# Performance work log

Measured on AMD Instinct MI355X. Metric: run time of the kernel, lower is better.

## Reference

```python
import jax, jax.numpy as jnp
import numpy as np

B, S, E = 2, 2048, 2048
H, HKV, D = 32, 8, 64  # n_heads, n_kv_heads, head_dim


def _rope(x, cos, sin):
    # x: [B,S,h,D]; cos/sin: [1,S,1,D//2]. Complex rotate on (even,odd) pairs.
    xp = x.reshape(*x.shape[:-1], D // 2, 2)
    x0, x1 = xp[..., 0], xp[..., 1]
    r0 = x0 * cos - x1 * sin
    r1 = x0 * sin + x1 * cos
    return jnp.stack([r0, r1], axis=-1).reshape(x.shape)


def setup_inputs() -> dict:
    key = jax.random.key(0)
    ks = jax.random.split(key, 8)
    sc = 0.02
    # real RoPE frequencies (theta=10000) for realism
    inv = 1.0 / (10000.0 ** (np.arange(0, D, 2, dtype=np.float32) / D))
    t = np.arange(S, dtype=np.float32)
    ang = np.outer(t, inv)  # [S, D/2]
    return {
        "x": jax.random.normal(ks[0], (B, S, E), jnp.float32),
        "start_pos": 0,
        "freqs_cos": jnp.asarray(np.cos(ang))[None, :, None, :],
        "freqs_sin": jnp.asarray(np.sin(ang))[None, :, None, :],
        "wq": jax.random.normal(ks[1], (E, H * D), jnp.float32) * sc,
        "wk": jax.random.normal(ks[2], (E, HKV * D), jnp.float32) * sc,
        "wv": jax.random.normal(ks[3], (E, HKV * D), jnp.float32) * sc,
        "out_w": jax.random.normal(ks[4], (H * D, E), jnp.float32) * sc,
        "out_b": jnp.zeros((E,), jnp.float32),
        "k_cache": jnp.zeros((B, S, HKV, D), jnp.float32),
        "v_cache": jnp.zeros((B, S, HKV, D), jnp.float32),
    }


def reference(x, start_pos, freqs_cos, freqs_sin, wq, wk, wv, out_w, out_b, k_cache, v_cache):
    b, s, _ = x.shape
    q = (x @ wq).reshape(b, s, H, D)
    k = (x @ wk).reshape(b, s, HKV, D)
    v = (x @ wv).reshape(b, s, HKV, D)
    q = _rope(q, freqs_cos[:, :s], freqs_sin[:, :s])
    k = _rope(k, freqs_cos[:, :s], freqs_sin[:, :s])
    # KV-cache append (torch code detaches before writing)
    k_cache = jax.lax.dynamic_update_slice(k_cache, jax.lax.stop_gradient(k), (0, start_pos, 0, 0))
    v_cache = jax.lax.dynamic_update_slice(v_cache, jax.lax.stop_gradient(v), (0, start_pos, 0, 0))
    keys = k_cache[:b, : start_pos + s]    # [b, T, HKV, D]
    values = v_cache[:b, : start_pos + s]
    g = H // HKV
    if g > 1:  # GQA head repeat
        keys = jnp.repeat(keys, g, axis=2)     # [b, T, H, D]
        values = jnp.repeat(values, g, axis=2)
    scores = jnp.einsum("bqhd,bkhd->bhqk", q, keys) / jnp.sqrt(jnp.float32(D))
    att = jax.nn.softmax(scores, axis=-1)  # NOTE: source applies no causal mask
    o = jnp.einsum("bhqk,bkhd->bqhd", att, values).reshape(b, s, H * D)
    return o @ out_w + out_b
```

## Files before the change

kernel.cpp:

```cpp
#include <hip/hip_runtime.h>
#include <math.h>

#define B_    2
#define S_    2048
#define E_    2048
#define H_    32
#define HKV_  8
#define D_    64

typedef __bf16 bf16x8 __attribute__((ext_vector_type(8)));
typedef float  f32x4  __attribute__((ext_vector_type(4)));
typedef float  f32x16 __attribute__((ext_vector_type(16)));
typedef unsigned int u32x2 __attribute__((ext_vector_type(2)));
typedef unsigned int u32x4 __attribute__((ext_vector_type(4)));

#define GPTR(x) ((const __attribute__((address_space(1))) void*)(x))
#define LPTR(x) ((__attribute__((address_space(3))) void*)(x))

#define QK_SCALE_LOG2E 0.18033688011112042f

__global__ __launch_bounds__(256) void convert_kernel(
    const float* __restrict__ in, __bf16* __restrict__ out, int n8)
{
    const int i = blockIdx.x * 256 + threadIdx.x;
    if (i >= n8) return;
    const float4 a = ((const float4*)in)[i * 2];
    const float4 b = ((const float4*)in)[i * 2 + 1];
    bf16x8 o;
    o[0] = (__bf16)a.x; o[1] = (__bf16)a.y; o[2] = (__bf16)a.z; o[3] = (__bf16)a.w;
    o[4] = (__bf16)b.x; o[5] = (__bf16)b.y; o[6] = (__bf16)b.z; o[7] = (__bf16)b.w;
    ((bf16x8*)out)[i] = o;
}

__global__ __launch_bounds__(256) void transpose_convert_all_kernel(
    const float* __restrict__ wq, const float* __restrict__ wk,
    const float* __restrict__ wv, const float* __restrict__ wo,
    __bf16* __restrict__ wT, __bf16* __restrict__ woT)
{
    const float* in; __bf16* out; int N, xb;
    const int x = blockIdx.x;
    if (x < 64)      { in = wq; out = wT;                        N = 2048; xb = x; }
    else if (x < 80) { in = wk; out = wT + (size_t)2048 * 2048;  N = 512;  xb = x - 64; }
    else if (x < 96) { in = wv; out = wT + (size_t)2560 * 2048;  N = 512;  xb = x - 80; }
    else             { in = wo; out = woT;                       N = 2048; xb = x - 96; }
    const int K = 2048;

    __shared__ float tile[32][33];
    const int k0 = blockIdx.y * 32, n0 = xb * 32;
    const int r  = threadIdx.x >> 3;
    const int c4 = (threadIdx.x & 7) * 4;
    const float4 v = *(const float4*)&in[(size_t)(k0 + r) * N + n0 + c4];
    tile[r][c4 + 0] = v.x; tile[r][c4 + 1] = v.y;
    tile[r][c4 + 2] = v.z; tile[r][c4 + 3] = v.w;
    __syncthreads();
    ushort4 o;
    __bf16 h0 = (__bf16)tile[c4 + 0][r]; o.x = __builtin_bit_cast(unsigned short, h0);
    __bf16 h1 = (__bf16)tile[c4 + 1][r]; o.y = __builtin_bit_cast(unsigned short, h1);
    __bf16 h2 = (__bf16)tile[c4 + 2][r]; o.z = __builtin_bit_cast(unsigned short, h2);
    __bf16 h3 = (__bf16)tile[c4 + 3][r]; o.w = __builtin_bit_cast(unsigned short, h3);
    *(ushort4*)&out[(size_t)(n0 + r) * K + k0 + c4] = o;
}

template<int BM, int BN> struct PG {
    static constexpr int BK     = 32;
    static constexpr int ASLOT  = BM * BK;
    static constexpr int BSLOT  = BN * BK;
    static constexpr int SLOT   = ASLOT + BSLOT;
    static constexpr int AINSTR = BM / 128;
    static constexpr int BINSTR = BN / 128;
    static constexpr int L      = AINSTR + BINSTR;
    static constexpr int MI     = BM / 32;
    static constexpr int NJ     = BN / 64;
};

template<int BM, int BN>
__device__ __forceinline__ void stage_tile(
    const __bf16* __restrict__ A, const __bf16* __restrict__ Bt,
    int m0, int n0, int K, int T, __bf16* sl, int t, int wbase)
{
    using G = PG<BM, BN>;
    const int k0   = T * G::BK;
    const int rsub = t >> 2;
    const int cp   = t & 3;
#pragma unroll
    for (int g = 0; g < G::AINSTR; ++g) {
        const int row = g * 128 + rsub;
        const int cl  = cp ^ ((row >> 1) & 3);
        __builtin_amdgcn_global_load_lds(
            GPTR(A + (size_t)(m0 + row) * K + k0 + cl * 8),
            LPTR(sl + (g * 512 + wbase) * 8), 16, 0, 0);
    }
#pragma unroll
    for (int g = 0; g < G::BINSTR; ++g) {
        const int row = g * 128 + rsub;
        const int cl  = cp ^ ((row >> 1) & 3);
        __builtin_amdgcn_global_load_lds(
            GPTR(Bt + (size_t)(n0 + row) * K + k0 + cl * 8),
            LPTR(sl + G::ASLOT + (g * 512 + wbase) * 8), 16, 0, 0);
    }
}

template<int BM, int BN>
__device__ __forceinline__ void compute_tile(
    const __bf16* sl, int wrow, int wcol, int col, int quad,
    f32x4 acc[PG<BM, BN>::MI][PG<BM, BN>::NJ])
{
    using G = PG<BM, BN>;
    bf16x8 af[G::MI], bfr[G::NJ];
#pragma unroll
    for (int i = 0; i < G::MI; ++i) {
        const int m = wrow + i * 16 + col;
        af[i] = *(const bf16x8*)&sl[m * 32 + ((quad ^ ((m >> 1) & 3)) * 8)];
    }
#pragma unroll
    for (int j = 0; j < G::NJ; ++j) {
        const int n = wcol + j * 16 + col;
        bfr[j] = *(const bf16x8*)&sl[G::ASLOT + n * 32 + ((quad ^ ((n >> 1) & 3)) * 8)];
    }
    __builtin_amdgcn_s_setprio(1);
#pragma unroll
    for (int i = 0; i < G::MI; ++i)
#pragma unroll
        for (int j = 0; j < G::NJ; ++j)
            acc[i][j] = __builtin_amdgcn_mfma_f32_16x16x32_bf16(
                af[i], bfr[j], acc[i][j], 0, 0, 0);
    __builtin_amdgcn_s_setprio(0);
}

template<int BM, int BN>
__device__ __forceinline__ void gemm_pipe_body(
    const __bf16* __restrict__ A, const __bf16* __restrict__ Bt,
    int m0, int n0, int K, __bf16* sL,
    f32x4 acc[PG<BM, BN>::MI][PG<BM, BN>::NJ])
{
    using G = PG<BM, BN>;
    const int t     = threadIdx.x;
    const int wbase = t & ~63;
    const int lane  = t & 63;
    const int col   = lane & 15;
    const int quad  = lane >> 4;
    const int w     = t >> 6;
    const int wrow  = (w >> 2) * (BM / 2);
    const int wcol  = (w & 3) * (BN / 4);
    const int NT    = K / G::BK;

    stage_tile<BM, BN>(A, Bt, m0, n0, K, 0, sL + 0 * G::SLOT, t, wbase);
    stage_tile<BM, BN>(A, Bt, m0, n0, K, 1, sL + 1 * G::SLOT, t, wbase);
    stage_tile<BM, BN>(A, Bt, m0, n0, K, 2, sL + 2 * G::SLOT, t, wbase);

    int T = 0;
#pragma unroll 1
    for (; T < NT - 3; ++T) {
        asm volatile("s_waitcnt vmcnt(%0)" :: "n"(2 * G::L) : "memory");
        __builtin_amdgcn_s_barrier();
        stage_tile<BM, BN>(A, Bt, m0, n0, K, T + 3, sL + ((T + 3) & 3) * G::SLOT, t, wbase);
        compute_tile<BM, BN>(sL + (T & 3) * G::SLOT, wrow, wcol, col, quad, acc);
    }
    asm volatile("s_waitcnt vmcnt(%0)" :: "n"(2 * G::L) : "memory");
    __builtin_amdgcn_s_barrier();
    compute_tile<BM, BN>(sL + (T & 3) * G::SLOT, wrow, wcol, col, quad, acc); ++T;
    asm volatile("s_waitcnt vmcnt(%0)" :: "n"(G::L) : "memory");
    __builtin_amdgcn_s_barrier();
    compute_tile<BM, BN>(sL + (T & 3) * G::SLOT, wrow, wcol, col, quad, acc); ++T;
    asm volatile("s_waitcnt vmcnt(0)" ::: "memory");
    __builtin_amdgcn_s_barrier();
    compute_tile<BM, BN>(sL + (T & 3) * G::SLOT, wrow, wcol, col, quad, acc);
}

__global__ __launch_bounds__(512, 2) void gemm_qkv_kernel(
    const __bf16* __restrict__ xb, const __bf16* __restrict__ wT,
    const float* __restrict__ fc, const float* __restrict__ fs,
    __bf16* __restrict__ qb, __bf16* __restrict__ kb, __bf16* __restrict__ vb)
{
    __shared__ __bf16 sL[4 * PG<128, 256>::SLOT];
    f32x4 acc[4][4];
#pragma unroll
    for (int i = 0; i < 4; ++i)
#pragma unroll
        for (int j = 0; j < 4; ++j) acc[i][j] = (f32x4){0.f, 0.f, 0.f, 0.f};

    const int lin     = blockIdx.x;
    const int logical = (lin & 7) * 48 + (lin >> 3);
    const int bx      = logical % 12;
    const int m0      = (logical / 12) * 128;
    const int n0      = bx * 256;

    gemm_pipe_body<128, 256>(xb, wT, m0, n0, E_, sL, acc);

    __bf16* Cp; int ldc, base;
    if (bx < 8)       { Cp = qb; ldc = H_ * D_;   base = 0;    }
    else if (bx < 10) { Cp = kb; ldc = HKV_ * D_; base = 2048; }
    else              { Cp = vb; ldc = HKV_ * D_; base = 2560; }
    const bool  doRope = (bx < 10);
    const float qsc    = (bx < 8) ? QK_SCALE_LOG2E : 1.0f;

    const int t    = threadIdx.x;
    const int lane = t & 63;
    const int col  = lane & 15;
    const int quad = lane >> 4;
    const int w    = t >> 6;
    const int wrow = (w >> 2) * 64;
    const int wcol = (w & 3) * 64;
#pragma unroll
    for (int i = 0; i < 4; ++i)
#pragma unroll
        for (int j = 0; j < 4; ++j)
#pragma unroll
            for (int r = 0; r < 4; ++r) {
                const int m  = m0 + wrow + i * 16 + quad * 4 + r;
                const int ng = n0 + wcol + j * 16 + col;
                float val = acc[i][j][r] * qsc;
                if (doRope) {
                    const int   s    = m & (S_ - 1);
                    const int   pair = (ng & 63) >> 1;
                    const float c    = fc[s * 32 + pair];
                    const float sn   = fs[s * 32 + pair];
                    const float oth  = __shfl_xor(val, 1);
                    val = (lane & 1) ? (oth * sn + val * c)
                                     : (val * c - oth * sn);
                }
                Cp[(size_t)m * ldc + (ng - base)] = (__bf16)val;
            }
}

__global__ __launch_bounds__(512, 2) void gemm_out_kernel(
    const __bf16* __restrict__ ob, const __bf16* __restrict__ woT,
    const float* __restrict__ bias, float* __restrict__ out)
{
    __shared__ __bf16 sL[4 * PG<256, 128>::SLOT];
    f32x4 acc[8][2];
#pragma unroll
    for (int i = 0; i < 8; ++i)
#pragma unroll
        for (int j = 0; j < 2; ++j) acc[i][j] = (f32x4){0.f, 0.f, 0.f, 0.f};

    const int lin     = blockIdx.x;
    const int logical = (lin & 7) * 32 + (lin >> 3);
    const int n0      = (logical % 16) * 128;
    const int m0      = (logical / 16) * 256;

    gemm_pipe_body<256, 128>(ob, woT, m0, n0, H_ * D_, sL, acc);

    const int t    = threadIdx.x;
    const int lane = t & 63;
    const int col  = lane & 15;
    const int quad = lane >> 4;
    const int w    = t >> 6;
    const int wrow = (w >> 2) * 128;
    const int wcol = (w & 3) * 32;
#pragma unroll
    for (int i = 0; i < 8; ++i)
#pragma unroll
        for (int j = 0; j < 2; ++j)
#pragma unroll
            for (int r = 0; r < 4; ++r) {
                const int m = m0 + wrow + i * 16 + quad * 4 + r;
                const int n = n0 + wcol + j * 16 + col;
                out[(size_t)m * E_ + n] = acc[i][j][r] + bias[n];
            }
}

struct StageRegs {
    bf16x8  k0, k1;
    ushort4 va0, vc0, va1, vc1;
};

__device__ __forceinline__ void stage_load(
    StageRegs& r, const __bf16* kbase, const __bf16* vbase, int j0,
    int kkey, int kd, int vkp, int vdg)
{
    const int KSTR = HKV_ * D_;
    const __bf16* kr = kbase + (size_t)(j0 + kkey) * KSTR + kd;
    r.k0 = ((const bf16x8*)kr)[0];
    r.k1 = ((const bf16x8*)kr)[1];
    const __bf16* v0 = vbase + (size_t)(j0 + vkp) * KSTR + vdg;
    r.va0 = *(const ushort4*)(v0);
    r.vc0 = *(const ushort4*)(v0 + KSTR);
    r.va1 = *(const ushort4*)(v0 + 32);
    r.vc1 = *(const ushort4*)(v0 + KSTR + 32);
}

__device__ __forceinline__ void stage_write(
    const StageRegs& r, __bf16 (*sK)[72], __bf16 (*sVT)[72],
    int kkey, int kd, int vkp, int vdg)
{
    *(bf16x8*)&sK[kkey][kd]     = r.k0;
    *(bf16x8*)&sK[kkey][kd + 8] = r.k1;
    *(unsigned int*)&sVT[vdg + 0][vkp]      = ((unsigned)r.vc0.x << 16) | r.va0.x;
    *(unsigned int*)&sVT[vdg + 1][vkp]      = ((unsigned)r.vc0.y << 16) | r.va0.y;
    *(unsigned int*)&sVT[vdg + 2][vkp]      = ((unsigned)r.vc0.z << 16) | r.va0.z;
    *(unsigned int*)&sVT[vdg + 3][vkp]      = ((unsigned)r.vc0.w << 16) | r.va0.w;
    *(unsigned int*)&sVT[vdg + 32 + 0][vkp] = ((unsigned)r.vc1.x << 16) | r.va1.x;
    *(unsigned int*)&sVT[vdg + 32 + 1][vkp] = ((unsigned)r.vc1.y << 16) | r.va1.y;
    *(unsigned int*)&sVT[vdg + 32 + 2][vkp] = ((unsigned)r.vc1.z << 16) | r.va1.z;
    *(unsigned int*)&sVT[vdg + 32 + 3][vkp] = ((unsigned)r.vc1.w << 16) | r.va1.w;
}

__device__ __forceinline__ bf16x8 pack_pa(const f32x16& p, int i0)
{
    unsigned a0, a1, a2, a3;
    asm("v_cvt_pk_bf16_f32 %0, %1, %2" : "=v"(a0) : "v"(p[i0 + 0]), "v"(p[i0 + 1]));
    asm("v_cvt_pk_bf16_f32 %0, %1, %2" : "=v"(a1) : "v"(p[i0 + 2]), "v"(p[i0 + 3]));
    asm("v_cvt_pk_bf16_f32 %0, %1, %2" : "=v"(a2) : "v"(p[i0 + 4]), "v"(p[i0 + 5]));
    asm("v_cvt_pk_bf16_f32 %0, %1, %2" : "=v"(a3) : "v"(p[i0 + 6]), "v"(p[i0 + 7]));
    const u32x2 s02 = __builtin_amdgcn_permlane32_swap(a0, a2, false, false);
    const u32x2 s13 = __builtin_amdgcn_permlane32_swap(a1, a3, false, false);
    return __builtin_bit_cast(bf16x8, (u32x4){s02[0], s13[0], s02[1], s13[1]});
}

__device__ __forceinline__ void attn_tile(
    const __bf16 (*sK)[72], const __bf16 (*sVT)[72],
    const bf16x8* bQ, int lq, int hi,
    f32x16& O0, f32x16& O1, float& lsum)
{
    f32x16 p0, p1;
#pragma unroll
    for (int i = 0; i < 16; ++i) { p0[i] = 0.f; p1[i] = 0.f; }
    __builtin_amdgcn_s_setprio(1);
#pragma unroll
    for (int ks = 0; ks < 4; ++ks) {
        const bf16x8 aK0 = *(const bf16x8*)&sK[lq][ks * 16 + hi * 8];
        const bf16x8 aK1 = *(const bf16x8*)&sK[32 + lq][ks * 16 + hi * 8];
        p0 = __builtin_amdgcn_mfma_f32_32x32x16_bf16(aK0, bQ[ks], p0, 0, 0, 0);
        p1 = __builtin_amdgcn_mfma_f32_32x32x16_bf16(aK1, bQ[ks], p1, 0, 0, 0);
    }
    __builtin_amdgcn_s_setprio(0);

    bf16x8 vbf[8];
#pragma unroll
    for (int ks = 0; ks < 4; ++ks) {
        vbf[ks * 2]     = *(const bf16x8*)&sVT[lq][ks * 16 + hi * 8];
        vbf[ks * 2 + 1] = *(const bf16x8*)&sVT[32 + lq][ks * 16 + hi * 8];
    }

    float ps = 0.f;
#pragma unroll
    for (int i = 0; i < 16; ++i) {
        p0[i] = __builtin_amdgcn_exp2f(p0[i]);
        p1[i] = __builtin_amdgcn_exp2f(p1[i]);
        ps += p0[i] + p1[i];
    }
    lsum += ps;

    bf16x8 pa[4];
    pa[0] = pack_pa(p0, 0);
    pa[1] = pack_pa(p0, 8);
    pa[2] = pack_pa(p1, 0);
    pa[3] = pack_pa(p1, 8);

    __builtin_amdgcn_s_setprio(1);
#pragma unroll
    for (int ks = 0; ks < 4; ++ks) {
        O0 = __builtin_amdgcn_mfma_f32_32x32x16_bf16(pa[ks], vbf[ks * 2],     O0, 0, 0, 0);
        O1 = __builtin_amdgcn_mfma_f32_32x32x16_bf16(pa[ks], vbf[ks * 2 + 1], O1, 0, 0, 0);
    }
    __builtin_amdgcn_s_setprio(0);
}

__global__ __launch_bounds__(256) void attn_kernel(
    const __bf16* __restrict__ qw, const __bf16* __restrict__ kw,
    const __bf16* __restrict__ vw, __bf16* __restrict__ ow)
{
    __shared__ __bf16 sK0[64][72], sVT0[64][72];
    __shared__ __bf16 sK1[64][72], sVT1[64][72];

    const int t    = threadIdx.x;
    const int lane = t & 63;
    const int w    = t >> 6;
    const int lq   = lane & 31;
    const int hi   = lane >> 5;

    const int bh  = blockIdx.y;
    const int b   = bh >> 5;
    const int h   = bh & 31;
    const int kvh = h >> 2;
    const int q0  = blockIdx.x * 128 + w * 32;

    bf16x8 bQ[4];
    {
        const __bf16* qrow = qw + (((size_t)b * S_ + q0 + lq) * H_ + h) * D_;
#pragma unroll
        for (int ks = 0; ks < 4; ++ks)
            bQ[ks] = *(const bf16x8*)(qrow + ks * 16 + hi * 8);
    }

    f32x16 O0, O1;
#pragma unroll
    for (int i = 0; i < 16; ++i) { O0[i] = 0.f; O1[i] = 0.f; }
    float lsum = 0.f;

    const __bf16* kbase = kw + ((size_t)b * S_ * HKV_ + kvh) * D_;
    const __bf16* vbase = vw + ((size_t)b * S_ * HKV_ + kvh) * D_;
    const int kkey = t >> 2,        kd  = (t & 3) * 16;
    const int vkp  = (t & 31) * 2,  vdg = (t >> 5) * 4;

    StageRegs sr;
    stage_load(sr, kbase, vbase, 0, kkey, kd, vkp, vdg);
    stage_write(sr, sK0, sVT0, kkey, kd, vkp, vdg);
    __syncthreads();

#pragma unroll 1
    for (int j0 = 0; j0 < S_; j0 += 128) {
        StageRegs nx;
        stage_load(nx, kbase, vbase, j0 + 64, kkey, kd, vkp, vdg);
        attn_tile(sK0, sVT0, bQ, lq, hi, O0, O1, lsum);
        stage_write(nx, sK1, sVT1, kkey, kd, vkp, vdg);
        __syncthreads();
        if (j0 + 128 < S_)
            stage_load(nx, kbase, vbase, j0 + 128, kkey, kd, vkp, vdg);
        attn_tile(sK1, sVT1, bQ, lq, hi, O0, O1, lsum);
        if (j0 + 128 < S_)
            stage_write(nx, sK0, sVT0, kkey, kd, vkp, vdg);
        __syncthreads();
    }

    lsum += __shfl_xor(lsum, 32);
    const float inv = 1.0f / lsum;

#pragma unroll
    for (int r = 0; r < 16; ++r) {
        const int   qr = (r & 3) + 8 * (r >> 2) + 4 * hi;
        const float li = __shfl(inv, qr);
        __bf16* orow = ow + (((size_t)b * S_ + q0 + qr) * H_ + h) * D_;
        orow[lq]      = (__bf16)(O0[r] * li);
        orow[32 + lq] = (__bf16)(O1[r] * li);
    }
}

extern "C" void kernel_launch(void* const* d_in, const int* in_sizes, int n_in,
                              void* d_out, int out_size, void* d_ws, size_t ws_size,
                              hipStream_t stream)
{
    const float* x  = (const float*)d_in[0];
    const float* fc = (const float*)d_in[2];
    const float* fs = (const float*)d_in[3];
    const float* wq = (const float*)d_in[4];
    const float* wk = (const float*)d_in[5];
    const float* wv = (const float*)d_in[6];
    const float* wo = (const float*)d_in[7];
    const float* obias = (const float*)d_in[8];
    float* out = (float*)d_out;

    __bf16* ws  = (__bf16*)d_ws;
    __bf16* xb  = ws;
    __bf16* wT  = xb  + (size_t)4096 * 2048;
    __bf16* woT = wT  + (size_t)3072 * 2048;
    __bf16* qb  = woT + (size_t)2048 * 2048;
    __bf16* kb  = qb  + (size_t)B_ * S_ * H_ * D_;
    __bf16* vb  = kb  + (size_t)B_ * S_ * HKV_ * D_;
    __bf16* obf = vb  + (size_t)B_ * S_ * HKV_ * D_;

    convert_kernel<<<4096, 256, 0, stream>>>(x, xb, 4096 * 2048 / 8);
    transpose_convert_all_kernel<<<dim3(160, 64), 256, 0, stream>>>(
        wq, wk, wv, wo, wT, woT);

    gemm_qkv_kernel<<<384, 512, 0, stream>>>(xb, wT, fc, fs, qb, kb, vb);

    attn_kernel<<<dim3(S_ / 128, B_ * H_), 256, 0, stream>>>(qb, kb, vb, obf);

    gemm_out_kernel<<<256, 512, 0, stream>>>(obf, woT, obias, out);
}
```

Measured before the change: 361.5 us.

## Switch GEMMs to BK=64 double-buffered pipeline and retile QKV to 256x192

```diff
diff --git a/kernel.cpp b/kernel.cpp
--- a/kernel.cpp
+++ b/kernel.cpp
@@ -61,165 +61,154 @@
     *(ushort4*)&out[(size_t)(n0 + r) * K + k0 + c4] = o;
 }
 
-template<int BM, int BN> struct PG {
-    static constexpr int BK     = 32;
-    static constexpr int ASLOT  = BM * BK;
-    static constexpr int BSLOT  = BN * BK;
-    static constexpr int SLOT   = ASLOT + BSLOT;
-    static constexpr int AINSTR = BM / 128;
-    static constexpr int BINSTR = BN / 128;
-    static constexpr int L      = AINSTR + BINSTR;
-    static constexpr int MI     = BM / 32;
-    static constexpr int NJ     = BN / 64;
+template<int BM, int BN> struct DB {
+    static constexpr int ASLOT = BM * 64;
+    static constexpr int BSLOT = BN * 64;
+    static constexpr int SLOT  = ASLOT + BSLOT;
+    static constexpr int AG    = BM / 64;
+    static constexpr int BG    = BN / 64;
+    static constexpr int MI    = BM / 32;
+    static constexpr int NJ    = BN / 64;
 };
 
 template<int BM, int BN>
-__device__ __forceinline__ void stage_tile(
+__device__ __forceinline__ void stage64(
     const __bf16* __restrict__ A, const __bf16* __restrict__ Bt,
-    int m0, int n0, int K, int T, __bf16* sl, int t, int wbase)
-{
-    using G = PG<BM, BN>;
-    const int k0   = T * G::BK;
-    const int rsub = t >> 2;
-    const int cp   = t & 3;
-#pragma unroll
-    for (int g = 0; g < G::AINSTR; ++g) {
-        const int row = g * 128 + rsub;
-        const int cl  = cp ^ ((row >> 1) & 3);
+    int m0, int n0, int K, int T, __bf16* sl, int t)
+{
+    using G = DB<BM, BN>;
+    const int k0 = T * 64;
+    const int rs = t >> 3;
+    const int cp = t & 7;
+#pragma unroll
+    for (int g = 0; g < G::AG; ++g) {
+        const int row = g * 64 + rs;
+        const int cs  = cp ^ (row & 7);
         __builtin_amdgcn_global_load_lds(
-            GPTR(A + (size_t)(m0 + row) * K + k0 + cl * 8),
-            LPTR(sl + (g * 512 + wbase) * 8), 16, 0, 0);
-    }
-#pragma unroll
-    for (int g = 0; g < G::BINSTR; ++g) {
-        const int row = g * 128 + rsub;
-        const int cl  = cp ^ ((row >> 1) & 3);
+            GPTR(A + (size_t)(m0 + row) * K + k0 + cs * 8),
+            LPTR(sl + g * 4096 + t * 8), 16, 0, 0);
+    }
+#pragma unroll
+    for (int g = 0; g < G::BG; ++g) {
+        const int row = g * 64 + rs;
+        const int cs  = cp ^ (row & 7);
         __builtin_amdgcn_global_load_lds(
-            GPTR(Bt + (size_t)(n0 + row) * K + k0 + cl * 8),
-            LPTR(sl + G::ASLOT + (g * 512 + wbase) * 8), 16, 0, 0);
+            GPTR(Bt + (size_t)(n0 + row) * K + k0 + cs * 8),
+            LPTR(sl + G::ASLOT + g * 4096 + t * 8), 16, 0, 0);
     }
 }
 
 template<int BM, int BN>
-__device__ __forceinline__ void compute_tile(
+__device__ __forceinline__ void compute64(
     const __bf16* sl, int wrow, int wcol, int col, int quad,
-    f32x4 acc[PG<BM, BN>::MI][PG<BM, BN>::NJ])
-{
-    using G = PG<BM, BN>;
-    bf16x8 af[G::MI], bfr[G::NJ];
-#pragma unroll
-    for (int i = 0; i < G::MI; ++i) {
-        const int m = wrow + i * 16 + col;
-        af[i] = *(const bf16x8*)&sl[m * 32 + ((quad ^ ((m >> 1) & 3)) * 8)];
-    }
-#pragma unroll
-    for (int j = 0; j < G::NJ; ++j) {
-        const int n = wcol + j * 16 + col;
-        bfr[j] = *(const bf16x8*)&sl[G::ASLOT + n * 32 + ((quad ^ ((n >> 1) & 3)) * 8)];
-    }
-    __builtin_amdgcn_s_setprio(1);
-#pragma unroll
-    for (int i = 0; i < G::MI; ++i)
-#pragma unroll
-        for (int j = 0; j < G::NJ; ++j)
-            acc[i][j] = __builtin_amdgcn_mfma_f32_16x16x32_bf16(
-                af[i], bfr[j], acc[i][j], 0, 0, 0);
-    __builtin_amdgcn_s_setprio(0);
+    f32x4 acc[DB<BM, BN>::MI][DB<BM, BN>::NJ])
+{
+    using G = DB<BM, BN>;
+#pragma unroll
+    for (int kk = 0; kk < 2; ++kk) {
+        bf16x8 af[G::MI], bfr[G::NJ];
+#pragma unroll
+        for (int i = 0; i < G::MI; ++i) {
+            const int m = wrow + i * 16 + col;
+            af[i] = *(const bf16x8*)&sl[m * 64 + (((kk * 4 + quad) ^ (m & 7)) * 8)];
+        }
+#pragma unroll
+        for (int j = 0; j < G::NJ; ++j) {
+            const int n = wcol + j * 16 + col;
+            bfr[j] = *(const bf16x8*)&sl[G::ASLOT + n * 64 + (((kk * 4 + quad) ^ (n & 7)) * 8)];
+        }
+        __builtin_amdgcn_s_setprio(1);
+#pragma unroll
+        for (int i = 0; i < G::MI; ++i)
+#pragma unroll
+            for (int j = 0; j < G::NJ; ++j)
+                acc[i][j] = __builtin_amdgcn_mfma_f32_16x16x32_bf16(
+                    af[i], bfr[j], acc[i][j], 0, 0, 0);
+        __builtin_amdgcn_s_setprio(0);
+    }
 }
 
 template<int BM, int BN>
-__device__ __forceinline__ void gemm_pipe_body(
+__device__ __forceinline__ void gemm_db_body(
     const __bf16* __restrict__ A, const __bf16* __restrict__ Bt,
     int m0, int n0, int K, __bf16* sL,
-    f32x4 acc[PG<BM, BN>::MI][PG<BM, BN>::NJ])
-{
-    using G = PG<BM, BN>;
-    const int t     = threadIdx.x;
-    const int wbase = t & ~63;
-    const int lane  = t & 63;
-    const int col   = lane & 15;
-    const int quad  = lane >> 4;
-    const int w     = t >> 6;
-    const int wrow  = (w >> 2) * (BM / 2);
-    const int wcol  = (w & 3) * (BN / 4);
-    const int NT    = K / G::BK;
-
-    stage_tile<BM, BN>(A, Bt, m0, n0, K, 0, sL + 0 * G::SLOT, t, wbase);
-    stage_tile<BM, BN>(A, Bt, m0, n0, K, 1, sL + 1 * G::SLOT, t, wbase);
-    stage_tile<BM, BN>(A, Bt, m0, n0, K, 2, sL + 2 * G::SLOT, t, wbase);
-
-    int T = 0;
-#pragma unroll 1
-    for (; T < NT - 3; ++T) {
-        asm volatile("s_waitcnt vmcnt(%0)" :: "n"(2 * G::L) : "memory");
-        __builtin_amdgcn_s_barrier();
-        stage_tile<BM, BN>(A, Bt, m0, n0, K, T + 3, sL + ((T + 3) & 3) * G::SLOT, t, wbase);
-        compute_tile<BM, BN>(sL + (T & 3) * G::SLOT, wrow, wcol, col, quad, acc);
-    }
-    asm volatile("s_waitcnt vmcnt(%0)" :: "n"(2 * G::L) : "memory");
-    __builtin_amdgcn_s_barrier();
-    compute_tile<BM, BN>(sL + (T & 3) * G::SLOT, wrow, wcol, col, quad, acc); ++T;
-    asm volatile("s_waitcnt vmcnt(%0)" :: "n"(G::L) : "memory");
-    __builtin_amdgcn_s_barrier();
-    compute_tile<BM, BN>(sL + (T & 3) * G::SLOT, wrow, wcol, col, quad, acc); ++T;
-    asm volatile("s_waitcnt vmcnt(0)" ::: "memory");
-    __builtin_amdgcn_s_barrier();
-    compute_tile<BM, BN>(sL + (T & 3) * G::SLOT, wrow, wcol, col, quad, acc);
-}
-
-__global__ __launch_bounds__(512, 2) void gemm_qkv_kernel(
-    const __bf16* __restrict__ xb, const __bf16* __restrict__ wT,
-    const float* __restrict__ fc, const float* __restrict__ fs,
-    __bf16* __restrict__ qb, __bf16* __restrict__ kb, __bf16* __restrict__ vb)
-{
-    __shared__ __bf16 sL[4 * PG<128, 256>::SLOT];
-    f32x4 acc[4][4];
-#pragma unroll
-    for (int i = 0; i < 4; ++i)
-#pragma unroll
-        for (int j = 0; j < 4; ++j) acc[i][j] = (f32x4){0.f, 0.f, 0.f, 0.f};
-
-    const int lin     = blockIdx.x;
-    const int logical = (lin & 7) * 48 + (lin >> 3);
-    const int bx      = logical % 12;
-    const int m0      = (logical / 12) * 128;
-    const int n0      = bx * 256;
-
-    gemm_pipe_body<128, 256>(xb, wT, m0, n0, E_, sL, acc);
-
-    __bf16* Cp; int ldc, base;
-    if (bx < 8)       { Cp = qb; ldc = H_ * D_;   base = 0;    }
-    else if (bx < 10) { Cp = kb; ldc = HKV_ * D_; base = 2048; }
-    else              { Cp = vb; ldc = HKV_ * D_; base = 2560; }
-    const bool  doRope = (bx < 10);
-    const float qsc    = (bx < 8) ? QK_SCALE_LOG2E : 1.0f;
-
+    f32x4 acc[DB<BM, BN>::MI][DB<BM, BN>::NJ])
+{
+    using G = DB<BM, BN>;
     const int t    = threadIdx.x;
     const int lane = t & 63;
     const int col  = lane & 15;
     const int quad = lane >> 4;
     const int w    = t >> 6;
-    const int wrow = (w >> 2) * 64;
-    const int wcol = (w & 3) * 64;
-#pragma unroll
-    for (int i = 0; i < 4; ++i)
-#pragma unroll
-        for (int j = 0; j < 4; ++j)
+    const int wrow = (w >> 2) * (BM / 2);
+    const int wcol = (w & 3) * (BN / 4);
+    const int NT   = K / 64;
+
+    stage64<BM, BN>(A, Bt, m0, n0, K, 0, sL, t);
+    asm volatile("s_waitcnt vmcnt(0)" ::: "memory");
+    __builtin_amdgcn_s_barrier();
+
+#pragma unroll 1
+    for (int T = 0; T < NT; ++T) {
+        if (T + 1 < NT)
+            stage64<BM, BN>(A, Bt, m0, n0, K, T + 1, sL + ((T + 1) & 1) * G::SLOT, t);
+        compute64<BM, BN>(sL + (T & 1) * G::SLOT, wrow, wcol, col, quad, acc);
+        asm volatile("s_waitcnt vmcnt(0)" ::: "memory");
+        __builtin_amdgcn_s_barrier();
+    }
+}
+
+__global__ __launch_bounds__(512, 2) void gemm_qkv_kernel(
+    const __bf16* __restrict__ xb, const __bf16* __restrict__ wT,
+    const float* __restrict__ fc, const float* __restrict__ fs,
+    __bf16* __restrict__ qb, __bf16* __restrict__ kb, __bf16* __restrict__ vb)
+{
+    __shared__ __bf16 sL[2 * DB<256, 192>::SLOT];
+    f32x4 acc[8][3];
+#pragma unroll
+    for (int i = 0; i < 8; ++i)
+#pragma unroll
+        for (int j = 0; j < 3; ++j) acc[i][j] = (f32x4){0.f, 0.f, 0.f, 0.f};
+
+    const int lin     = blockIdx.x;
+    const int logical = (lin & 7) * 32 + (lin >> 3);
+    const int m0      = (logical >> 4) * 256;
+    const int n0      = (logical & 15) * 192;
+
+    gemm_db_body<256, 192>(xb, wT, m0, n0, E_, sL, acc);
+
+    const int t    = threadIdx.x;
+    const int lane = t & 63;
+    const int col  = lane & 15;
+    const int quad = lane >> 4;
+    const int w    = t >> 6;
+    const int wrow = (w >> 2) * 128;
+    const int wcol = (w & 3) * 48;
+#pragma unroll
+    for (int i = 0; i < 8; ++i)
+#pragma unroll
+        for (int j = 0; j < 3; ++j)
 #pragma unroll
             for (int r = 0; r < 4; ++r) {
-                const int m  = m0 + wrow + i * 16 + quad * 4 + r;
-                const int ng = n0 + wcol + j * 16 + col;
-                float val = acc[i][j][r] * qsc;
-                if (doRope) {
+                const int m = m0 + wrow + i * 16 + quad * 4 + r;
+                const int n = n0 + wcol + j * 16 + col;
+                float val = acc[i][j][r];
+                if (n < 2560) {
+                    if (n < 2048) val *= QK_SCALE_LOG2E;
                     const int   s    = m & (S_ - 1);
-                    const int   pair = (ng & 63) >> 1;
+                    const int   pair = (n & 63) >> 1;
                     const float c    = fc[s * 32 + pair];
                     const float sn   = fs[s * 32 + pair];
                     const float oth  = __shfl_xor(val, 1);
                     val = (lane & 1) ? (oth * sn + val * c)
                                      : (val * c - oth * sn);
                 }
-                Cp[(size_t)m * ldc + (ng - base)] = (__bf16)val;
+                if (n < 2048)
+                    qb[(size_t)m * (H_ * D_) + n] = (__bf16)val;
+                else if (n < 2560)
+                    kb[(size_t)m * (HKV_ * D_) + (n - 2048)] = (__bf16)val;
+                else
+                    vb[(size_t)m * (HKV_ * D_) + (n - 2560)] = (__bf16)val;
             }
 }
 
@@ -227,7 +216,7 @@
     const __bf16* __restrict__ ob, const __bf16* __restrict__ woT,
     const float* __restrict__ bias, float* __restrict__ out)
 {
-    __shared__ __bf16 sL[4 * PG<256, 128>::SLOT];
+    __shared__ __bf16 sL[2 * DB<256, 128>::SLOT];
     f32x4 acc[8][2];
 #pragma unroll
     for (int i = 0; i < 8; ++i)
@@ -239,7 +228,7 @@
     const int n0      = (logical % 16) * 128;
     const int m0      = (logical / 16) * 256;
 
-    gemm_pipe_body<256, 128>(ob, woT, m0, n0, H_ * D_, sL, acc);
+    gemm_db_body<256, 128>(ob, woT, m0, n0, H_ * D_, sL, acc);
 
     const int t    = threadIdx.x;
     const int lane = t & 63;
@@ -454,7 +443,7 @@
     transpose_convert_all_kernel<<<dim3(160, 64), 256, 0, stream>>>(
         wq, wk, wv, wo, wT, woT);
 
-    gemm_qkv_kernel<<<384, 512, 0, stream>>>(xb, wT, fc, fs, qb, kb, vb);
+    gemm_qkv_kernel<<<256, 512, 0, stream>>>(xb, wT, fc, fs, qb, kb, vb);
 
     attn_kernel<<<dim3(S_ / 128, B_ * H_), 256, 0, stream>>>(qb, kb, vb, obf);
 
```

After: 347.5 us. -3.9%, faster.
